# Kernel tuning notes

Measured on AMD Instinct MI355X. Metric: run time of the kernel, lower is better.

The kernel has to match this reference:

```python
import jax, jax.numpy as jnp
import numpy as np

B = 512          # batch
IN_BITS = 1024   # raw input bit width
N_IN = 4096      # input-layer neurons
N_ST = 2048      # state-layer neurons
N_OUT = 2048     # output-layer neurons
K = 14           # bits (connections) per neuron
TABLE = 1 << K   # 16384 memory words per neuron


def setup_inputs() -> dict:
    key = jax.random.key(0)
    ks = jax.random.split(key, 8)
    x = jax.random.bernoulli(ks[0], 0.5, (B, IN_BITS))                       # bool input bits
    state = jnp.zeros((B, N_ST), dtype=bool)                                 # reset_state() -> zeros
    # random wiring: each neuron reads K positions of its layer's input vector
    in_conn = jax.random.randint(ks[1], (N_IN, K), 0, IN_BITS)
    st_conn = jax.random.randint(ks[2], (N_ST, K), 0, N_IN + N_ST)
    out_conn = jax.random.randint(ks[3], (N_OUT, K), 0, N_IN + N_ST)
    # RAM memory tables: one boolean word per (neuron, address)
    in_mem = jax.random.bernoulli(ks[4], 0.5, (N_IN, TABLE))
    st_mem = jax.random.bernoulli(ks[5], 0.5, (N_ST, TABLE))
    out_mem = jax.random.bernoulli(ks[6], 0.5, (N_OUT, TABLE))
    return dict(x=x, state=state, in_conn=in_conn, st_conn=st_conn,
                out_conn=out_conn, in_mem=in_mem, st_mem=st_mem, out_mem=out_mem)


def _ram_layer(bits, conn, mem):
    """bits: [B, T] bool; conn: [N, K] int; mem: [N, 2^K] -> [B, N] lookup."""
    g = bits[:, conn].astype(jnp.int32)                      # [B, N, K] gathered bits
    weights = (jnp.int32(1) << jnp.arange(K, dtype=jnp.int32))  # 2^k address weights
    addr = jnp.sum(g * weights, axis=-1)                     # [B, N] RAM addresses
    n_idx = jnp.arange(mem.shape[0], dtype=jnp.int32)[None, :]
    return mem[n_idx, addr]                                  # [B, N]


def reference(x, state, in_conn, st_conn, out_conn, in_mem, st_mem, out_mem):
    # input_layer(input)
    h = _ram_layer(x, in_conn, in_mem)                       # [B, N_IN] bool
    # state_layer(cat(input_layer_output, prev_state))
    s = _ram_layer(jnp.concatenate([h, state], axis=1), st_conn, st_mem)   # [B, N_ST]
    # output_layer(cat(input_layer_output, current_state))
    out = _ram_layer(jnp.concatenate([h, s], axis=1), out_conn, out_mem)   # [B, N_OUT]
    return out
```

## Files before the change

kernel.cpp:

```cpp
#include <hip/hip_runtime.h>

#define BATCH 512
#define KBITS 14
#define TABLE 16384

__global__ void transpose_pack(const int* __restrict__ in,
                               unsigned char* __restrict__ out,
                               int C) {
    int idx = blockIdx.x * blockDim.x + threadIdx.x;
    if (idx >= BATCH * C) return;
    int b = idx / C;
    int c = idx - b * C;
    out[(size_t)c * BATCH + b] = (unsigned char)(in[idx] & 1);
}

__global__ __launch_bounds__(128)
void ram_layer(const unsigned char* __restrict__ in0,
               const unsigned char* __restrict__ in1,
               int split,
               const int* __restrict__ conn,
               const int* __restrict__ mem,
               unsigned char* __restrict__ outT)
{
    const int n = blockIdx.x;
    const int b0 = threadIdx.x * 4;

    const int* cp = conn + n * KBITS;

    unsigned int a0 = 0, a1 = 0, a2 = 0, a3 = 0;
#pragma unroll
    for (int k = 0; k < KBITS; ++k) {
        int c = cp[k];
        const unsigned char* row = (c < split) ? (in0 + (size_t)c * BATCH)
                                               : (in1 + (size_t)(c - split) * BATCH);
        unsigned int w = *(const unsigned int*)(row + b0);
        a0 += ((w      ) & 1u) << k;
        a1 += ((w >>  8) & 1u) << k;
        a2 += ((w >> 16) & 1u) << k;
        a3 += ((w >> 24) & 1u) << k;
    }

    const int* m = mem + (size_t)n * TABLE;
    uchar4 r;
    r.x = (unsigned char)(m[a0] & 1);
    r.y = (unsigned char)(m[a1] & 1);
    r.z = (unsigned char)(m[a2] & 1);
    r.w = (unsigned char)(m[a3] & 1);
    *(uchar4*)(outT + (size_t)n * BATCH + b0) = r;
}

__global__ void out_convert(const unsigned char* __restrict__ oT,
                            int* __restrict__ out, int N) {
    int idx = blockIdx.x * blockDim.x + threadIdx.x;
    if (idx >= BATCH * N) return;
    int b = idx / N;
    int n = idx - b * N;
    out[idx] = (int)(oT[(size_t)n * BATCH + b] & 1);
}

extern "C" void kernel_launch(void* const* d_in, const int* in_sizes, int n_in,
                              void* d_out, int out_size, void* d_ws, size_t ws_size,
                              hipStream_t stream) {
    const int* x        = (const int*)d_in[0];
    const int* state    = (const int*)d_in[1];
    const int* in_conn  = (const int*)d_in[2];
    const int* st_conn  = (const int*)d_in[3];
    const int* out_conn = (const int*)d_in[4];
    const int* in_mem   = (const int*)d_in[5];
    const int* st_mem   = (const int*)d_in[6];
    const int* out_mem  = (const int*)d_in[7];
    int* out = (int*)d_out;

    unsigned char* ws  = (unsigned char*)d_ws;
    unsigned char* xT  = ws;
    unsigned char* hsT = ws + 524288;
    unsigned char* sT  = ws + 524288 + 3145728;
    unsigned char* oT  = ws + 524288 + 3145728 + 1048576;

    transpose_pack<<<(512 * 1024) / 256, 256, 0, stream>>>(x, xT, 1024);
    transpose_pack<<<(512 * 2048) / 256, 256, 0, stream>>>(state, hsT + (size_t)4096 * 512, 2048);

    ram_layer<<<4096, 128, 0, stream>>>(xT, xT, 1 << 30, in_conn, in_mem, hsT);
    ram_layer<<<2048, 128, 0, stream>>>(hsT, hsT, 1 << 30, st_conn, st_mem, sT);
    ram_layer<<<2048, 128, 0, stream>>>(hsT, sT, 4096, out_conn, out_mem, oT);

    out_convert<<<(BATCH * 2048) / 256, 256, 0, stream>>>(oT, out, 2048);
}
```

Measured before the change: 76.29 us.

## Bit-pack activations to one bit per batch element and tile the transposes

Activations are stored bit-packed, 64 bytes per neuron for the 512-element batch, in place of one byte per element. This cuts the bytes read for each gathered connection row by a factor of eight. Each RAM-layer thread now forms 8 addresses from 14 byte loads, and the kernel runs two neurons per block. The input transposes use an LDS-tiled kernel that packs bits, and the output conversion unpacks them. The trade is extra bit-manipulation ALU work and fewer threads per neuron, while the random memory-table lookups that likely dominate stay the same.

```diff
diff --git a/kernel.cpp b/kernel.cpp
--- a/kernel.cpp
+++ b/kernel.cpp
@@ -4,58 +4,82 @@
 #define KBITS 14
 #define TABLE 16384
 
-__global__ void transpose_pack(const int* __restrict__ in,
-                               unsigned char* __restrict__ out,
-                               int C) {
-    int idx = blockIdx.x * blockDim.x + threadIdx.x;
-    if (idx >= BATCH * C) return;
-    int b = idx / C;
-    int c = idx - b * C;
-    out[(size_t)c * BATCH + b] = (unsigned char)(in[idx] & 1);
+
+__global__ __launch_bounds__(256)
+void tp_pack(const int* __restrict__ in, unsigned char* __restrict__ out, int C) {
+    __shared__ unsigned char lds[64 * 65];
+    const int c0 = blockIdx.x * 64;
+    const int b0 = blockIdx.y * 64;
+    const int t = threadIdx.x;
+
+#pragma unroll
+    for (int i = 0; i < 16; ++i) {
+        int flat = i * 256 + t;
+        int brow = flat >> 6;
+        int ccol = flat & 63;
+        lds[ccol * 65 + brow] = (unsigned char)(in[(size_t)(b0 + brow) * C + (c0 + ccol)] & 1);
+    }
+    __syncthreads();
+
+    const int c = t >> 2;
+    const int q = t & 3;
+#pragma unroll
+    for (int jj = 0; jj < 2; ++jj) {
+        int j = q * 2 + jj;
+        unsigned int byte = 0;
+#pragma unroll
+        for (int i = 0; i < 8; ++i)
+            byte |= ((unsigned int)lds[c * 65 + j * 8 + i] & 1u) << i;
+        out[(size_t)(c0 + c) * 64 + (b0 >> 3) + j] = (unsigned char)byte;
+    }
 }
 
 __global__ __launch_bounds__(128)
-void ram_layer(const unsigned char* __restrict__ in0,
-               const unsigned char* __restrict__ in1,
-               int split,
-               const int* __restrict__ conn,
-               const int* __restrict__ mem,
-               unsigned char* __restrict__ outT)
+void ram_layer_p(const unsigned char* __restrict__ in0,
+                 const unsigned char* __restrict__ in1,
+                 int split,
+                 const int* __restrict__ conn,
+                 const int* __restrict__ mem,
+                 unsigned char* __restrict__ outP)
 {
-    const int n = blockIdx.x;
-    const int b0 = threadIdx.x * 4;
-
+    const int n = blockIdx.x * 2 + (threadIdx.x >> 6);
+    const int t = threadIdx.x & 63;
     const int* cp = conn + n * KBITS;
 
-    unsigned int a0 = 0, a1 = 0, a2 = 0, a3 = 0;
+    unsigned char w[KBITS];
 #pragma unroll
     for (int k = 0; k < KBITS; ++k) {
         int c = cp[k];
-        const unsigned char* row = (c < split) ? (in0 + (size_t)c * BATCH)
-                                               : (in1 + (size_t)(c - split) * BATCH);
-        unsigned int w = *(const unsigned int*)(row + b0);
-        a0 += ((w      ) & 1u) << k;
-        a1 += ((w >>  8) & 1u) << k;
-        a2 += ((w >> 16) & 1u) << k;
-        a3 += ((w >> 24) & 1u) << k;
+        const unsigned char* row = (c < split) ? (in0 + (size_t)c * 64)
+                                               : (in1 + (size_t)(c - split) * 64);
+        w[k] = row[t];
+    }
+
+    unsigned int a[8] = {0, 0, 0, 0, 0, 0, 0, 0};
+#pragma unroll
+    for (int k = 0; k < KBITS; ++k) {
+#pragma unroll
+        for (int j = 0; j < 8; ++j)
+            a[j] |= (((unsigned int)w[k] >> j) & 1u) << k;
     }
 
     const int* m = mem + (size_t)n * TABLE;
-    uchar4 r;
-    r.x = (unsigned char)(m[a0] & 1);
-    r.y = (unsigned char)(m[a1] & 1);
-    r.z = (unsigned char)(m[a2] & 1);
-    r.w = (unsigned char)(m[a3] & 1);
-    *(uchar4*)(outT + (size_t)n * BATCH + b0) = r;
+    int r[8];
+#pragma unroll
+    for (int j = 0; j < 8; ++j) r[j] = m[a[j]];
+    unsigned int res = 0;
+#pragma unroll
+    for (int j = 0; j < 8; ++j) res |= ((unsigned int)r[j] & 1u) << j;
+
+    outP[(size_t)n * 64 + t] = (unsigned char)res;
 }
 
-__global__ void out_convert(const unsigned char* __restrict__ oT,
-                            int* __restrict__ out, int N) {
+__global__ __launch_bounds__(256)
+void out_convert_p(const unsigned char* __restrict__ oP, int* __restrict__ out) {
     int idx = blockIdx.x * blockDim.x + threadIdx.x;
-    if (idx >= BATCH * N) return;
-    int b = idx / N;
-    int n = idx - b * N;
-    out[idx] = (int)(oT[(size_t)n * BATCH + b] & 1);
+    int b = idx >> 11;
+    int n = idx & 2047;
+    out[idx] = (oP[(size_t)n * 64 + (b >> 3)] >> (b & 7)) & 1;
 }
 
 extern "C" void kernel_launch(void* const* d_in, const int* in_sizes, int n_in,
@@ -72,17 +96,19 @@
     int* out = (int*)d_out;
 
     unsigned char* ws  = (unsigned char*)d_ws;
-    unsigned char* xT  = ws;
-    unsigned char* hsT = ws + 524288;
-    unsigned char* sT  = ws + 524288 + 3145728;
-    unsigned char* oT  = ws + 524288 + 3145728 + 1048576;
+    unsigned char* xP  = ws;
+    unsigned char* hsP = ws + (64 << 10);
+    unsigned char* sP  = ws + (448 << 10);
+    unsigned char* oP  = ws + (576 << 10);
 
-    transpose_pack<<<(512 * 1024) / 256, 256, 0, stream>>>(x, xT, 1024);
-    transpose_pack<<<(512 * 2048) / 256, 256, 0, stream>>>(state, hsT + (size_t)4096 * 512, 2048);
+    dim3 gx(1024 / 64, 512 / 64);
+    tp_pack<<<gx, 256, 0, stream>>>(x, xP, 1024);
+    dim3 gs(2048 / 64, 512 / 64);
+    tp_pack<<<gs, 256, 0, stream>>>(state, hsP + (size_t)4096 * 64, 2048);
 
-    ram_layer<<<4096, 128, 0, stream>>>(xT, xT, 1 << 30, in_conn, in_mem, hsT);
-    ram_layer<<<2048, 128, 0, stream>>>(hsT, hsT, 1 << 30, st_conn, st_mem, sT);
-    ram_layer<<<2048, 128, 0, stream>>>(hsT, sT, 4096, out_conn, out_mem, oT);
+    ram_layer_p<<<4096 / 2, 128, 0, stream>>>(xP, xP, 1 << 30, in_conn, in_mem, hsP);
+    ram_layer_p<<<2048 / 2, 128, 0, stream>>>(hsP, hsP, 1 << 30, st_conn, st_mem, sP);
+    ram_layer_p<<<2048 / 2, 128, 0, stream>>>(hsP, sP, 4096, out_conn, out_mem, oP);
 
-    out_convert<<<(BATCH * 2048) / 256, 256, 0, stream>>>(oT, out, 2048);
+    out_convert_p<<<(BATCH * 2048) / 256, 256, 0, stream>>>(oP, out);
 }
```

Result: faster. 66.51 us (-12.8%).
